# Performance work log

Measured on AMD Instinct MI355X. Metric: run time of the kernel, lower is better.

## Reference

```python
import jax, jax.numpy as jnp
import numpy as np

H = 224          # image height (self.shape[0])
W_IMG = 224      # image width (self.shape[1])
CELLS = 7        # mask_generator num_cells
PAD = CELLS // 2 # reflect pad size
D = 512          # encoder feature dim
NUM_BATCHES = 30
BATCH = 100
EPS = 1e-8       # torch CosineSimilarity eps


def _encode(xb, Wenc):
    # stand-in encoder: 32x32 block average pool -> [B,3,7,7] -> linear to D
    B = xb.shape[0]
    feats = xb.reshape(B, 3, CELLS, H // CELLS, CELLS, W_IMG // CELLS).mean(axis=(3, 5))
    return feats.reshape(B, -1) @ Wenc  # [B, D]


def _cosine(a, b):
    # a: [1,D] (h_star), b: [B,D]; matches nn.CosineSimilarity(dim=1)
    num = jnp.sum(a * b, axis=1)
    den = jnp.maximum(jnp.linalg.norm(a, axis=1) * jnp.linalg.norm(b, axis=1), EPS)
    return num / den  # [B]


def _make_masks(grid, sx, sy):
    # grid: [B,1,7,7] binary floats; bilinear upsample, reflect pad, shifted crop
    B = grid.shape[0]
    up = jax.image.resize(grid, (B, 1, H, W_IMG), method='linear')
    padded = jnp.pad(up, ((0, 0), (0, 0), (PAD, PAD), (PAD, PAD)), mode='reflect')
    crop = jax.vmap(
        lambda g, i, j: jax.lax.dynamic_slice(g, (0, i, j), (1, H, W_IMG))
    )(padded, sx, sy)
    return crop  # [B,1,H,W]


def _relax(x, Wenc, grids, shifts_x, shifts_y):
    h_star = _encode(x, Wenc)  # [1, D]
    R0 = jnp.zeros((H, W_IMG), jnp.float32)
    U0 = jnp.zeros_like(R0)
    sow0 = jnp.full((H, W_IMG), 1e-10, jnp.float32)

    def sample_step(carry, inp):
        # sequential weighted running-mean / Welford variance update
        R, U, sow = carry
        s, m = inp  # s: scalar sim, m: [H,W] mask
        sow = sow + m
        R_new = R + m * (s - R) / sow
        U = U + (s - R_new) * (s - R) * m
        return (R_new, U, sow), None

    def batch_step(carry, binp):
        grid, sx, sy = binp
        masks = _make_masks(grid, sx, sy)        # [B,1,H,W]
        x_mask = x * masks                       # fill_vals_zeros=True path
        h = _encode(x_mask, Wenc)                # [B,D]
        sims = _cosine(h_star, h)                # [B]
        carry, _ = jax.lax.scan(sample_step, carry, (sims, masks[:, 0]))
        return carry, None

    (R, U, sow), _ = jax.lax.scan(batch_step, (R0, U0, sow0),
                                  (grids, shifts_x, shifts_y))
    uncertainty = U / (sow - 1.0)
    return jnp.stack([R, uncertainty])  # [2,H,W]: importance, uncertainty


def setup_inputs() -> dict:
    key = jax.random.key(0)
    k1, k2, k3, k4, k5 = jax.random.split(key, 5)
    x = jax.random.normal(k1, (1, 3, H, W_IMG), jnp.float32)
    Wenc = jax.random.normal(k2, (3 * CELLS * CELLS, D), jnp.float32) * 0.05
    grids = (jax.random.uniform(k3, (NUM_BATCHES, BATCH, 1, CELLS, CELLS)) < 0.5).astype(jnp.float32)
    shifts_x = jax.random.randint(k4, (NUM_BATCHES, BATCH), 0, CELLS)
    shifts_y = jax.random.randint(k5, (NUM_BATCHES, BATCH), 0, CELLS)
    return {"x": x, "Wenc": Wenc, "grids": grids,
            "shifts_x": shifts_x, "shifts_y": shifts_y}


def reference(x, Wenc, grids, shifts_x, shifts_y):
    return _relax(x, Wenc, grids, shifts_x, shifts_y)
```

## Files before the change

### kernel.cpp

```cpp
#include <hip/hip_runtime.h>
#include <math.h>

#define NS 3000
#define NF 147
#define ND 512
#define NSIG 49
#define NSAMP 4
#define NHBLK 750

#define OFF_WT     0
#define OFF_FEATS  6272
#define OFF_V      6432
#define OFF_T      236928
#define OFF_G      589952

__device__ __forceinline__ void wt_compute(int sigma, int p, int& i0c, int& i1c,
                                           float& w0, float& w1) {
  int k = p + sigma - 3;
  int r = k < 0 ? -k : (k > 223 ? 446 - k : k);
  float tc = (float)(2 * r - 31) * (1.0f / 64.0f);
  float fl = floorf(tc);
  int i0 = (int)fl;
  float fr = tc - fl;
  i0c = min(max(i0, 0), 6);
  i1c = min(max(i0 + 1, 0), 6);
  w0 = 1.0f - fr;
  w1 = fr;
}

__global__ void __launch_bounds__(256) k_initV(const float* __restrict__ x,
                                               float* __restrict__ ws) {
  int b = blockIdx.x;
  int t = threadIdx.x;
  if (b < NF) {
    int c = b / 49, rem = b % 49, cy = rem / 7, cx = rem % 7;
    float acc = 0.f;
    for (int idx = t; idx < 1024; idx += 256) {
      int yy = idx >> 5, xx = idx & 31;
      acc += x[(c * 224 + cy * 32 + yy) * 224 + cx * 32 + xx];
    }
    for (int off = 32; off; off >>= 1) acc += __shfl_down(acc, off);
    __shared__ float red[4];
    int wave = t >> 6, lane = t & 63;
    if (lane == 0) red[wave] = acc;
    __syncthreads();
    if (t == 0) ws[OFF_FEATS + b] = (red[0] + red[1] + red[2] + red[3]) * (1.0f / 1024.0f);
  } else if (b == NF) {
    float4* WT = (float4*)(ws + OFF_WT);
    for (int e = t; e < 7 * 224; e += 256) {
      int sigma = e / 224, p = e % 224;
      int i0c, i1c; float w0, w1;
      wt_compute(sigma, p, i0c, i1c, w0, w1);
      WT[e] = make_float4(w0, w1, __int_as_float(i0c), __int_as_float(i1c));
    }
  } else {
    int tid = (b - NF - 1) * 256 + t;
    if (tid >= 7 * 3 * 224 * 7) return;
    int cx = tid % 7;
    int y  = (tid / 7) % 224;
    int c  = (tid / (7 * 224)) % 3;
    int sy = tid / (7 * 224 * 3);
    float acc[7];
    #pragma unroll
    for (int g = 0; g < 7; ++g) acc[g] = 0.f;
    const float* xrow = x + (c * 224 + y) * 224;
    for (int x0 = 0; x0 < 32; ++x0) {
      int px = cx * 32 + x0;
      int i0, i1; float w0, w1;
      wt_compute(sy, px, i0, i1, w0, w1);
      float v = xrow[px];
      #pragma unroll
      for (int g = 0; g < 7; ++g) {
        float w = (g == i0 ? w0 : 0.f) + (g == i1 ? w1 : 0.f);
        acc[g] = fmaf(w, v, acc[g]);
      }
    }
    float* Vp = ws + OFF_V + (((sy * 3 + c) * 224 + y) * 49 + cx * 7);
    #pragma unroll
    for (int g = 0; g < 7; ++g) Vp[g] = acc[g];
  }
}

__global__ void __launch_bounds__(256) k_T(float* __restrict__ ws) {
  int tid = blockIdx.x * blockDim.x + threadIdx.x;
  if (tid >= NSIG * NF * 49) {
    int e = tid - NSIG * NF * 49;
    if (e < 7203) ws[OFF_G + e] = 0.f;
    return;
  }
  int g = tid % 49;
  int f = (tid / 49) % NF;
  int sig = tid / (49 * NF);
  int sx = sig / 7, sy = sig % 7;
  int gy = g / 7, gx = g % 7;
  int c = f / 49, rem = f % 49, cy = rem / 7, cx = rem % 7;
  const float4* WT = (const float4*)(ws + OFF_WT);
  const float* V = ws + OFF_V + ((sy * 3 + c) * 224) * 49 + cx * 7 + gx;
  float acc = 0.f;
  for (int y0 = 0; y0 < 32; ++y0) {
    int y = cy * 32 + y0;
    float4 wt = WT[sx * 224 + y];
    int i0 = __float_as_int(wt.z), i1 = __float_as_int(wt.w);
    float w = (gy == i0 ? wt.x : 0.f) + (gy == i1 ? wt.y : 0.f);
    acc = fmaf(w, V[y * 49], acc);
  }
  ws[OFF_T + (sig * 49 + g) * NF + f] = acc * (1.0f / 1024.0f);
}

__global__ void __launch_bounds__(256) k_H2s(const float* __restrict__ Wenc,
                                             const float* __restrict__ grids,
                                             const int* __restrict__ shx,
                                             const int* __restrict__ shy,
                                             float* __restrict__ ws) {
  __shared__ __align__(16) float sF[NF * NSAMP];
  __shared__ float sGr[NSAMP * 49];
  __shared__ float sFeat[NF];
  __shared__ int   sSig[NSAMP];
  __shared__ float sRed[2][NSAMP][4];
  __shared__ float sRedH[4];
  __shared__ float sS[NSAMP];
  int t = threadIdx.x;
  int b = blockIdx.x;
  int i0s = b * NSAMP;
  for (int e = t; e < NSAMP * 49; e += 256) sGr[e] = grids[i0s * 49 + e];
  if (t < NSAMP) sSig[t] = shx[i0s + t] * 7 + shy[i0s + t];
  if (t < NF) sFeat[t] = ws[OFF_FEATS + t];
  __syncthreads();
  for (int idx = t; idx < NF * NSAMP; idx += 256) {
    int r = idx / NF, f = idx - r * NF;
    const float* T2 = ws + OFF_T + sSig[r] * (49 * NF) + f;
    const float* gr = sGr + r * 49;
    float acc = 0.f;
    #pragma unroll
    for (int g = 0; g < 49; ++g) acc = fmaf(T2[g * NF], gr[g], acc);
    sF[f * NSAMP + r] = acc;
  }
  __syncthreads();
  float accA[NSAMP], accB[NSAMP];
  #pragma unroll
  for (int r = 0; r < NSAMP; ++r) { accA[r] = 0.f; accB[r] = 0.f; }
  float h0 = 0.f, h1 = 0.f;
  const float* W0 = Wenc + t;
  const float* W1 = Wenc + t + 256;
  const float4* sF4 = (const float4*)sF;
  for (int f = 0; f < NF; ++f) {
    float w0 = W0[f * ND];
    float w1 = W1[f * ND];
    float fe = sFeat[f];
    h0 = fmaf(fe, w0, h0);
    h1 = fmaf(fe, w1, h1);
    float4 a4 = sF4[f];
    float a[NSAMP] = {a4.x, a4.y, a4.z, a4.w};
    #pragma unroll
    for (int r = 0; r < NSAMP; ++r) {
      accA[r] = fmaf(a[r], w0, accA[r]);
      accB[r] = fmaf(a[r], w1, accB[r]);
    }
  }
  int wave = t >> 6, lane = t & 63;
  float hq = h0 * h0 + h1 * h1;
  for (int off = 32; off; off >>= 1) hq += __shfl_down(hq, off);
  if (lane == 0) sRedH[wave] = hq;
  #pragma unroll
  for (int r = 0; r < NSAMP; ++r) {
    float np = accA[r] * h0 + accB[r] * h1;
    float sp = accA[r] * accA[r] + accB[r] * accB[r];
    for (int off = 32; off; off >>= 1) {
      np += __shfl_down(np, off);
      sp += __shfl_down(sp, off);
    }
    if (lane == 0) { sRed[0][r][wave] = np; sRed[1][r][wave] = sp; }
  }
  __syncthreads();
  if (t == 0) sRedH[0] = sqrtf(sRedH[0] + sRedH[1] + sRedH[2] + sRedH[3]);
  __syncthreads();
  if (t < NSAMP) {
    float np = sRed[0][t][0] + sRed[0][t][1] + sRed[0][t][2] + sRed[0][t][3];
    float sp = sRed[1][t][0] + sRed[1][t][1] + sRed[1][t][2] + sRed[1][t][3];
    float den = fmaxf(sRedH[0] * sqrtf(sp), 1e-8f);
    sS[t] = np / den;
  }
  __syncthreads();
  for (int e = t; e < NSAMP * 3 * 49; e += 256) {
    int k = e % 49;
    int rp = e / 49;
    int r = rp / 3, p = rp - r * 3;
    float gv = sGr[r * 49 + k];
    if (gv != 0.f) {
      float s = sS[r];
      float add = (p == 0) ? 1.f : ((p == 1) ? s : s * s);
      atomicAdd(&ws[OFF_G + p * 2401 + sSig[r] * 49 + k], add);
    }
  }
}

__global__ void __launch_bounds__(256) k_CO(const float* __restrict__ ws,
                                            float* __restrict__ out) {
  __shared__ float Gl[3 * 2401];
  __shared__ float sC[NF];
  int b = blockIdx.x;
  int t = threadIdx.x;
  for (int e = t; e < 3 * 2401; e += 256) Gl[e] = ws[OFF_G + e];
  __syncthreads();
  const float4* WT = (const float4*)(ws + OFF_WT);
  if (t < NF) {
    int k = t / 49, r = t - k * 49;
    int sx = r / 7, gy = r % 7;
    float acc = 0.f;
    for (int sy = 0; sy < 7; ++sy) {
      float4 wt = WT[sy * 224 + b];
      int i0 = __float_as_int(wt.z), i1 = __float_as_int(wt.w);
      int base = k * 2401 + (sx * 7 + sy) * 49 + gy * 7;
      acc += wt.x * Gl[base + i0] + wt.y * Gl[base + i1];
    }
    sC[t] = acc;
  }
  __syncthreads();
  if (t < 224) {
    int py = t;
    float S0 = 0.f, S1 = 0.f, S2 = 0.f;
    for (int sx = 0; sx < 7; ++sx) {
      float4 wt = WT[sx * 224 + py];
      int i0 = __float_as_int(wt.z), i1 = __float_as_int(wt.w);
      int base = sx * 7;
      S0 += wt.x * sC[base + i0]      + wt.y * sC[base + i1];
      S1 += wt.x * sC[49 + base + i0] + wt.y * sC[49 + base + i1];
      S2 += wt.x * sC[98 + base + i0] + wt.y * sC[98 + base + i1];
    }
    float W = 1e-10f + S0;
    float R = S1 / W;
    float U = S2 - S1 * S1 / W;
    out[py * 224 + b] = R;
    out[224 * 224 + py * 224 + b] = U / (W - 1.0f);
  }
}

extern "C" void kernel_launch(void* const* d_in, const int* in_sizes, int n_in,
                              void* d_out, int out_size, void* d_ws, size_t ws_size,
                              hipStream_t stream) {
  const float* x     = (const float*)d_in[0];
  const float* Wenc  = (const float*)d_in[1];
  const float* grids = (const float*)d_in[2];
  const int*   shx   = (const int*)d_in[3];
  const int*   shy   = (const int*)d_in[4];
  float* out = (float*)d_out;
  float* ws  = (float*)d_ws;

  int vblocks = (7 * 3 * 224 * 7 + 255) / 256;
  k_initV<<<NF + 1 + vblocks, 256, 0, stream>>>(x, ws);
  k_T<<<(NSIG * NF * 49 + 7203 + 255) / 256, 256, 0, stream>>>(ws);
  k_H2s<<<NHBLK, 256, 0, stream>>>(Wenc, grids, shx, shy, ws);
  k_CO<<<224, 256, 0, stream>>>(ws, out);
}
```

Measured before the change: 109.7 us.

## Fuse separable T-tensor precompute into one shared-memory kernel and widen encoder blocks

Merges the V and T precompute kernels into a single kernel. Each block stages a 32-row image strip in shared memory and does both separable bilinear contractions on-chip, so the global V intermediate and one kernel launch go away. The weight table is now computed inline instead of read from a precomputed table. The encoder kernel moves to 512 threads, with one output column per thread instead of two. The trade-off is redundant image loads across the 49 shift blocks and heavier shared-memory use per block.

```diff
diff --git a/kernel.cpp b/kernel.cpp
--- a/kernel.cpp
+++ b/kernel.cpp
@@ -7,12 +7,11 @@
 #define NSIG 49
 #define NSAMP 4
 #define NHBLK 750
-
-#define OFF_WT     0
-#define OFF_FEATS  6272
-#define OFF_V      6432
-#define OFF_T      236928
-#define OFF_G      589952
+#define NTB 1029
+
+#define OFF_FEATS  0
+#define OFF_T      160
+#define OFF_G      353120
 
 __device__ __forceinline__ void wt_compute(int sigma, int p, int& i0c, int& i1c,
                                            float& w0, float& w1) {
@@ -28,86 +27,86 @@
   w1 = fr;
 }
 
-__global__ void __launch_bounds__(256) k_initV(const float* __restrict__ x,
-                                               float* __restrict__ ws) {
+__global__ void __launch_bounds__(256) k_TX(const float* __restrict__ x,
+                                            float* __restrict__ ws) {
+  __shared__ float sImg[32 * 224];
+  __shared__ float4 sWx[224];
+  __shared__ float4 sWy[32];
+  __shared__ float sV[32 * 49];
+  __shared__ float red[4];
   int b = blockIdx.x;
   int t = threadIdx.x;
-  if (b < NF) {
-    int c = b / 49, rem = b % 49, cy = rem / 7, cx = rem % 7;
+  if (b < NTB) {
+    int cy = b % 7;
+    int c  = (b / 7) % 3;
+    int sig = b / 21;
+    int sx = sig / 7, sy = sig % 7;
+    const float* xc = x + (c * 224 + cy * 32) * 224;
+    for (int e = t; e < 32 * 224; e += 256) {
+      int yy = e / 224, col = e % 224;
+      int cx = col >> 5, x0 = col & 31;
+      sImg[yy * 224 + x0 * 7 + cx] = xc[yy * 224 + col];
+    }
+    if (t < 224) {
+      int i0, i1; float w0, w1;
+      wt_compute(sy, t, i0, i1, w0, w1);
+      sWx[(t & 31) * 7 + (t >> 5)] =
+          make_float4(w0, w1, __int_as_float(i0), __int_as_float(i1));
+    }
+    if (t < 32) {
+      int i0, i1; float w0, w1;
+      wt_compute(sx, cy * 32 + t, i0, i1, w0, w1);
+      sWy[t] = make_float4(w0, w1, __int_as_float(i0), __int_as_float(i1));
+    }
+    __syncthreads();
+    for (int e = t; e < 32 * 49; e += 256) {
+      int yy = e / 49, j = e % 49;
+      int cx = j / 7, gx = j % 7;
+      const float* row = sImg + yy * 224 + cx;
+      float acc = 0.f;
+      #pragma unroll 8
+      for (int x0 = 0; x0 < 32; ++x0) {
+        float4 wt = sWx[x0 * 7 + cx];
+        int i0 = __float_as_int(wt.z), i1 = __float_as_int(wt.w);
+        float w = (gx == i0 ? wt.x : 0.f) + (gx == i1 ? wt.y : 0.f);
+        acc = fmaf(w, row[x0 * 7], acc);
+      }
+      sV[e] = acc;
+    }
+    __syncthreads();
+    for (int e = t; e < 343; e += 256) {
+      int g = e / 7, cx = e % 7;
+      int gy = g / 7, gx = g % 7;
+      float acc = 0.f;
+      #pragma unroll 8
+      for (int yy = 0; yy < 32; ++yy) {
+        float4 wt = sWy[yy];
+        int i0 = __float_as_int(wt.z), i1 = __float_as_int(wt.w);
+        float w = (gy == i0 ? wt.x : 0.f) + (gy == i1 ? wt.y : 0.f);
+        acc = fmaf(w, sV[yy * 49 + cx * 7 + gx], acc);
+      }
+      ws[OFF_T + (sig * 49 + g) * NF + c * 49 + cy * 7 + cx] = acc * (1.0f / 1024.0f);
+    }
+  } else if (b < NTB + NF) {
+    int unit = b - NTB;
+    int c = unit / 49, rem = unit % 49, cy = rem / 7, cx = rem % 7;
     float acc = 0.f;
     for (int idx = t; idx < 1024; idx += 256) {
       int yy = idx >> 5, xx = idx & 31;
       acc += x[(c * 224 + cy * 32 + yy) * 224 + cx * 32 + xx];
     }
     for (int off = 32; off; off >>= 1) acc += __shfl_down(acc, off);
-    __shared__ float red[4];
     int wave = t >> 6, lane = t & 63;
     if (lane == 0) red[wave] = acc;
     __syncthreads();
-    if (t == 0) ws[OFF_FEATS + b] = (red[0] + red[1] + red[2] + red[3]) * (1.0f / 1024.0f);
-  } else if (b == NF) {
-    float4* WT = (float4*)(ws + OFF_WT);
-    for (int e = t; e < 7 * 224; e += 256) {
-      int sigma = e / 224, p = e % 224;
-      int i0c, i1c; float w0, w1;
-      wt_compute(sigma, p, i0c, i1c, w0, w1);
-      WT[e] = make_float4(w0, w1, __int_as_float(i0c), __int_as_float(i1c));
-    }
+    if (t == 0)
+      ws[OFF_FEATS + unit] = (red[0] + red[1] + red[2] + red[3]) * (1.0f / 1024.0f);
   } else {
-    int tid = (b - NF - 1) * 256 + t;
-    if (tid >= 7 * 3 * 224 * 7) return;
-    int cx = tid % 7;
-    int y  = (tid / 7) % 224;
-    int c  = (tid / (7 * 224)) % 3;
-    int sy = tid / (7 * 224 * 3);
-    float acc[7];
-    #pragma unroll
-    for (int g = 0; g < 7; ++g) acc[g] = 0.f;
-    const float* xrow = x + (c * 224 + y) * 224;
-    for (int x0 = 0; x0 < 32; ++x0) {
-      int px = cx * 32 + x0;
-      int i0, i1; float w0, w1;
-      wt_compute(sy, px, i0, i1, w0, w1);
-      float v = xrow[px];
-      #pragma unroll
-      for (int g = 0; g < 7; ++g) {
-        float w = (g == i0 ? w0 : 0.f) + (g == i1 ? w1 : 0.f);
-        acc[g] = fmaf(w, v, acc[g]);
-      }
-    }
-    float* Vp = ws + OFF_V + (((sy * 3 + c) * 224 + y) * 49 + cx * 7);
-    #pragma unroll
-    for (int g = 0; g < 7; ++g) Vp[g] = acc[g];
-  }
-}
-
-__global__ void __launch_bounds__(256) k_T(float* __restrict__ ws) {
-  int tid = blockIdx.x * blockDim.x + threadIdx.x;
-  if (tid >= NSIG * NF * 49) {
-    int e = tid - NSIG * NF * 49;
-    if (e < 7203) ws[OFF_G + e] = 0.f;
-    return;
-  }
-  int g = tid % 49;
-  int f = (tid / 49) % NF;
-  int sig = tid / (49 * NF);
-  int sx = sig / 7, sy = sig % 7;
-  int gy = g / 7, gx = g % 7;
-  int c = f / 49, rem = f % 49, cy = rem / 7, cx = rem % 7;
-  const float4* WT = (const float4*)(ws + OFF_WT);
-  const float* V = ws + OFF_V + ((sy * 3 + c) * 224) * 49 + cx * 7 + gx;
-  float acc = 0.f;
-  for (int y0 = 0; y0 < 32; ++y0) {
-    int y = cy * 32 + y0;
-    float4 wt = WT[sx * 224 + y];
-    int i0 = __float_as_int(wt.z), i1 = __float_as_int(wt.w);
-    float w = (gy == i0 ? wt.x : 0.f) + (gy == i1 ? wt.y : 0.f);
-    acc = fmaf(w, V[y * 49], acc);
-  }
-  ws[OFF_T + (sig * 49 + g) * NF + f] = acc * (1.0f / 1024.0f);
-}
-
-__global__ void __launch_bounds__(256) k_H2s(const float* __restrict__ Wenc,
+    for (int e = t; e < 7203; e += 256) ws[OFF_G + e] = 0.f;
+  }
+}
+
+__global__ void __launch_bounds__(512) k_H2s(const float* __restrict__ Wenc,
                                              const float* __restrict__ grids,
                                              const int* __restrict__ shx,
                                              const int* __restrict__ shy,
@@ -116,17 +115,17 @@
   __shared__ float sGr[NSAMP * 49];
   __shared__ float sFeat[NF];
   __shared__ int   sSig[NSAMP];
-  __shared__ float sRed[2][NSAMP][4];
-  __shared__ float sRedH[4];
+  __shared__ float sRed[2][NSAMP][8];
+  __shared__ float sRedH[8];
   __shared__ float sS[NSAMP];
   int t = threadIdx.x;
   int b = blockIdx.x;
   int i0s = b * NSAMP;
-  for (int e = t; e < NSAMP * 49; e += 256) sGr[e] = grids[i0s * 49 + e];
+  for (int e = t; e < NSAMP * 49; e += 512) sGr[e] = grids[i0s * 49 + e];
   if (t < NSAMP) sSig[t] = shx[i0s + t] * 7 + shy[i0s + t];
   if (t < NF) sFeat[t] = ws[OFF_FEATS + t];
   __syncthreads();
-  for (int idx = t; idx < NF * NSAMP; idx += 256) {
+  for (int idx = t; idx < NF * NSAMP; idx += 512) {
     int r = idx / NF, f = idx - r * NF;
     const float* T2 = ws + OFF_T + sSig[r] * (49 * NF) + f;
     const float* gr = sGr + r * 49;
@@ -136,35 +135,27 @@
     sF[f * NSAMP + r] = acc;
   }
   __syncthreads();
-  float accA[NSAMP], accB[NSAMP];
-  #pragma unroll
-  for (int r = 0; r < NSAMP; ++r) { accA[r] = 0.f; accB[r] = 0.f; }
-  float h0 = 0.f, h1 = 0.f;
-  const float* W0 = Wenc + t;
-  const float* W1 = Wenc + t + 256;
+  float a0 = 0.f, a1 = 0.f, a2 = 0.f, a3 = 0.f, h = 0.f;
+  const float* W = Wenc + t;
   const float4* sF4 = (const float4*)sF;
   for (int f = 0; f < NF; ++f) {
-    float w0 = W0[f * ND];
-    float w1 = W1[f * ND];
-    float fe = sFeat[f];
-    h0 = fmaf(fe, w0, h0);
-    h1 = fmaf(fe, w1, h1);
+    float w = W[f * ND];
+    h = fmaf(sFeat[f], w, h);
     float4 a4 = sF4[f];
-    float a[NSAMP] = {a4.x, a4.y, a4.z, a4.w};
-    #pragma unroll
-    for (int r = 0; r < NSAMP; ++r) {
-      accA[r] = fmaf(a[r], w0, accA[r]);
-      accB[r] = fmaf(a[r], w1, accB[r]);
-    }
+    a0 = fmaf(a4.x, w, a0);
+    a1 = fmaf(a4.y, w, a1);
+    a2 = fmaf(a4.z, w, a2);
+    a3 = fmaf(a4.w, w, a3);
   }
   int wave = t >> 6, lane = t & 63;
-  float hq = h0 * h0 + h1 * h1;
+  float hq = h * h;
   for (int off = 32; off; off >>= 1) hq += __shfl_down(hq, off);
   if (lane == 0) sRedH[wave] = hq;
+  float aA[NSAMP] = {a0, a1, a2, a3};
   #pragma unroll
   for (int r = 0; r < NSAMP; ++r) {
-    float np = accA[r] * h0 + accB[r] * h1;
-    float sp = accA[r] * accA[r] + accB[r] * accB[r];
+    float np = aA[r] * h;
+    float sp = aA[r] * aA[r];
     for (int off = 32; off; off >>= 1) {
       np += __shfl_down(np, off);
       sp += __shfl_down(sp, off);
@@ -172,16 +163,19 @@
     if (lane == 0) { sRed[0][r][wave] = np; sRed[1][r][wave] = sp; }
   }
   __syncthreads();
-  if (t == 0) sRedH[0] = sqrtf(sRedH[0] + sRedH[1] + sRedH[2] + sRedH[3]);
-  __syncthreads();
   if (t < NSAMP) {
-    float np = sRed[0][t][0] + sRed[0][t][1] + sRed[0][t][2] + sRed[0][t][3];
-    float sp = sRed[1][t][0] + sRed[1][t][1] + sRed[1][t][2] + sRed[1][t][3];
-    float den = fmaxf(sRedH[0] * sqrtf(sp), 1e-8f);
+    float hs = 0.f, np = 0.f, sp = 0.f;
+    #pragma unroll
+    for (int w8 = 0; w8 < 8; ++w8) {
+      hs += sRedH[w8];
+      np += sRed[0][t][w8];
+      sp += sRed[1][t][w8];
+    }
+    float den = fmaxf(sqrtf(hs) * sqrtf(sp), 1e-8f);
     sS[t] = np / den;
   }
   __syncthreads();
-  for (int e = t; e < NSAMP * 3 * 49; e += 256) {
+  for (int e = t; e < NSAMP * 3 * 49; e += 512) {
     int k = e % 49;
     int rp = e / 49;
     int r = rp / 3, p = rp - r * 3;
@@ -202,16 +196,15 @@
   int t = threadIdx.x;
   for (int e = t; e < 3 * 2401; e += 256) Gl[e] = ws[OFF_G + e];
   __syncthreads();
-  const float4* WT = (const float4*)(ws + OFF_WT);
   if (t < NF) {
     int k = t / 49, r = t - k * 49;
     int sx = r / 7, gy = r % 7;
     float acc = 0.f;
     for (int sy = 0; sy < 7; ++sy) {
-      float4 wt = WT[sy * 224 + b];
-      int i0 = __float_as_int(wt.z), i1 = __float_as_int(wt.w);
+      int i0, i1; float w0, w1;
+      wt_compute(sy, b, i0, i1, w0, w1);
       int base = k * 2401 + (sx * 7 + sy) * 49 + gy * 7;
-      acc += wt.x * Gl[base + i0] + wt.y * Gl[base + i1];
+      acc += w0 * Gl[base + i0] + w1 * Gl[base + i1];
     }
     sC[t] = acc;
   }
@@ -220,12 +213,12 @@
     int py = t;
     float S0 = 0.f, S1 = 0.f, S2 = 0.f;
     for (int sx = 0; sx < 7; ++sx) {
-      float4 wt = WT[sx * 224 + py];
-      int i0 = __float_as_int(wt.z), i1 = __float_as_int(wt.w);
+      int i0, i1; float w0, w1;
+      wt_compute(sx, py, i0, i1, w0, w1);
       int base = sx * 7;
-      S0 += wt.x * sC[base + i0]      + wt.y * sC[base + i1];
-      S1 += wt.x * sC[49 + base + i0] + wt.y * sC[49 + base + i1];
-      S2 += wt.x * sC[98 + base + i0] + wt.y * sC[98 + base + i1];
+      S0 += w0 * sC[base + i0]      + w1 * sC[base + i1];
+      S1 += w0 * sC[49 + base + i0] + w1 * sC[49 + base + i1];
+      S2 += w0 * sC[98 + base + i0] + w1 * sC[98 + base + i1];
     }
     float W = 1e-10f + S0;
     float R = S1 / W;
@@ -246,9 +239,7 @@
   float* out = (float*)d_out;
   float* ws  = (float*)d_ws;
 
-  int vblocks = (7 * 3 * 224 * 7 + 255) / 256;
-  k_initV<<<NF + 1 + vblocks, 256, 0, stream>>>(x, ws);
-  k_T<<<(NSIG * NF * 49 + 7203 + 255) / 256, 256, 0, stream>>>(ws);
-  k_H2s<<<NHBLK, 256, 0, stream>>>(Wenc, grids, shx, shy, ws);
+  k_TX<<<NTB + NF + 1, 256, 0, stream>>>(x, ws);
+  k_H2s<<<NHBLK, 512, 0, stream>>>(Wenc, grids, shx, shy, ws);
   k_CO<<<224, 256, 0, stream>>>(ws, out);
 }
```

Measured after the change: 112.9 us. 2.9% more time.
